# Kernel optimization log

Hardware: AMD Instinct MI355X
Metric: run time of the kernel (lower is better)

## Reference

```python
import jax, jax.numpy as jnp
import numpy as np

C = 256       # in_channels
IC = 128      # inter_channels = C // 2
G = 4         # num_group
D = IC // G   # per-group channels = 32
B, H, W_ = 4, 56, 56
EPS = 1e-5


def conv1x1(x, w, b=None):
    # x: (B,Cin,H,W), w: (Cout,Cin)
    y = jnp.einsum('bchw,oc->bohw', x, w)
    if b is not None:
        y = y + b[None, :, None, None]
    return y


def bn(x, scale, bias, mean, var):
    inv = scale / jnp.sqrt(var + EPS)
    return x * inv[None, :, None, None] + (bias - mean * inv)[None, :, None, None]


def setup_inputs():
    key = jax.random.key(0)
    ks = jax.random.split(key, 16)
    r = lambda k, shape, s=0.05: jax.random.normal(k, shape, jnp.float32) * s
    C4 = C // 4
    return {
        'x': jax.random.normal(ks[0], (B, C, H, W_), jnp.float32),
        'g_w': r(ks[1], (IC, C)), 'g_b': r(ks[2], (IC,)),
        'theta_w': r(ks[3], (IC, C)), 'theta_b': r(ks[4], (IC,)),
        'phi_w': r(ks[5], (IC, C)), 'phi_b': r(ks[6], (IC,)),
        'W_w': r(ks[7], (C, IC)), 'W_b': r(ks[8], (C,)),
        'bnW_scale': jnp.ones((C,)), 'bnW_bias': jnp.zeros((C,)),
        'bnW_mean': jnp.zeros((C,)), 'bnW_var': jnp.ones((C,)),
        'ff1_w': r(ks[9], (C4, C)),
        'ffbn1_scale': jnp.ones((C4,)), 'ffbn1_bias': jnp.zeros((C4,)),
        'ffbn1_mean': jnp.zeros((C4,)), 'ffbn1_var': jnp.ones((C4,)),
        'ff2_w': r(ks[10], (C4, C4, 3, 3)),
        'ffbn2_scale': jnp.ones((C4,)), 'ffbn2_bias': jnp.zeros((C4,)),
        'ffbn2_mean': jnp.zeros((C4,)), 'ffbn2_var': jnp.ones((C4,)),
        'ff3_w': r(ks[11], (C, C4)),
        'ffbn3_scale': jnp.ones((C,)), 'ffbn3_bias': jnp.zeros((C,)),
        'ffbn3_mean': jnp.zeros((C,)), 'ffbn3_var': jnp.ones((C,)),
    }


def reference(x, g_w, g_b, theta_w, theta_b, phi_w, phi_b, W_w, W_b,
              bnW_scale, bnW_bias, bnW_mean, bnW_var,
              ff1_w, ffbn1_scale, ffbn1_bias, ffbn1_mean, ffbn1_var,
              ff2_w, ffbn2_scale, ffbn2_bias, ffbn2_mean, ffbn2_var,
              ff3_w, ffbn3_scale, ffbn3_bias, ffbn3_mean, ffbn3_var):
    b, c, h, w = x.shape
    n = h * w
    # grouped non-local attention: channels split into G groups of D
    gx = conv1x1(x, g_w, g_b).reshape(b, G, D, n)       # (B,G,D,N)
    tx = conv1x1(x, theta_w, theta_b).reshape(b, G, D, n)
    px = conv1x1(x, phi_w, phi_b).reshape(b, G, D, n)
    f = jnp.einsum('bgdn,bgdm->bgnm', tx, px)           # (B,G,N,N) scores
    attn = jax.nn.softmax(f, axis=-1)                   # softmax over keys (torch dim=2 on (b,N,N))
    yy = jnp.einsum('bgnm,bgdm->bgdn', attn, gx)        # (B,G,D,N)
    y_out = yy.reshape(b, IC, h, w)
    W_y = bn(conv1x1(y_out, W_w, W_b), bnW_scale, bnW_bias, bnW_mean, bnW_var)
    z = jax.nn.relu(W_y + x)
    # FPNFFConv bottleneck FFN (BN in eval mode)
    o = jax.nn.relu(bn(conv1x1(z, ff1_w), ffbn1_scale, ffbn1_bias, ffbn1_mean, ffbn1_var))
    o = jax.lax.conv_general_dilated(o, ff2_w, (1, 1), 'SAME',
                                     dimension_numbers=('NCHW', 'OIHW', 'NCHW'))
    o = jax.nn.relu(bn(o, ffbn2_scale, ffbn2_bias, ffbn2_mean, ffbn2_var))
    o = bn(conv1x1(o, ff3_w), ffbn3_scale, ffbn3_bias, ffbn3_mean, ffbn3_var)
    return jax.nn.relu(o + z)
```

## Files before the change

kernel.cpp:

```cpp
#include <hip/hip_runtime.h>
#include <hip/hip_bf16.h>

#define NPIX 3136
#define BB 4
#define NSPLIT 5
#define LOG2E 1.4426950408889634f
#define ZLS 264

typedef unsigned short u16;
typedef __bf16 bf16x8 __attribute__((ext_vector_type(8)));
typedef float f32x4 __attribute__((ext_vector_type(4)));

__device__ __forceinline__ float b2f(u16 u) {
  union { unsigned u; float f; } c; c.u = ((unsigned)u) << 16; return c.f;
}
__device__ __forceinline__ u16 f2b(float f) {
  __hip_bfloat16 h = __float2bfloat16(f);
  return *reinterpret_cast<u16*>(&h);
}
__device__ __forceinline__ unsigned pk2(float a, float b) {
  return (unsigned)f2b(a) | ((unsigned)f2b(b) << 16);
}
__device__ __forceinline__ f32x4 mfma(bf16x8 a, bf16x8 b, f32x4 c) {
  return __builtin_amdgcn_mfma_f32_16x16x32_bf16(a, b, c, 0, 0, 0);
}
__device__ __forceinline__ float fast_exp2(float x) {
#if __has_builtin(__builtin_amdgcn_exp2f)
  return __builtin_amdgcn_exp2f(x);
#else
  float r; asm("v_exp_f32 %0, %1" : "=v"(r) : "v"(x)); return r;
#endif
}

template<int NSTEP, int NOT>
__device__ __forceinline__ void mf_gemm2(const u16* __restrict__ A0,
                                         const u16* __restrict__ A1,
                                         const u16* __restrict__ Brow, int sB,
                                         int lq, f32x4* acc) {
#pragma unroll
  for (int s = 0; s < NSTEP; ++s) {
    bf16x8 bf[NOT];
#pragma unroll
    for (int ot = 0; ot < NOT; ++ot)
      bf[ot] = *(const bf16x8*)(Brow + (size_t)ot * 16 * sB + s * 32 + lq * 8);
    bf16x8 a0 = *(const bf16x8*)(A0 + s * 32 + lq * 8);
    bf16x8 a1 = *(const bf16x8*)(A1 + s * 32 + lq * 8);
#pragma unroll
    for (int ot = 0; ot < NOT; ++ot) {
      acc[ot] = mfma(a0, bf[ot], acc[ot]);
      acc[NOT + ot] = mfma(a1, bf[ot], acc[NOT + ot]);
    }
  }
}

__global__ __launch_bounds__(256) void prep_w(
    const float* __restrict__ gw, const float* __restrict__ tw,
    const float* __restrict__ pw, const float* __restrict__ Ww,
    const float* __restrict__ f1w, const float* __restrict__ f2w,
    const float* __restrict__ f3w,
    u16* __restrict__ gwb, u16* __restrict__ twb, u16* __restrict__ pwb,
    u16* __restrict__ Wwb, u16* __restrict__ f1b, u16* __restrict__ f3b,
    u16* __restrict__ f2p) {
  for (int i = blockIdx.x * 256 + threadIdx.x; i < 200704; i += gridDim.x * 256) {
    int j = i;
    if (j < 32768) { gwb[j] = f2b(gw[j]); continue; } j -= 32768;
    if (j < 32768) { twb[j] = f2b(tw[j] * LOG2E); continue; } j -= 32768;
    if (j < 32768) { pwb[j] = f2b(pw[j]); continue; } j -= 32768;
    if (j < 32768) { Wwb[j] = f2b(Ww[j]); continue; } j -= 32768;
    if (j < 16384) { f1b[j] = f2b(f1w[j]); continue; } j -= 16384;
    if (j < 16384) { f3b[j] = f2b(f3w[j]); continue; } j -= 16384;
    int t = j >> 12, rem = j & 4095, co = rem >> 6, ci = rem & 63;
    f2p[j] = f2b(f2w[(co * 64 + ci) * 9 + t]);
  }
}

__global__ __launch_bounds__(256) void prep_x(const float* __restrict__ x,
                                              u16* __restrict__ xt) {
  __shared__ u16 sT[64 * 65];
  const int b = blockIdx.z, c0 = blockIdx.y * 64, n0 = blockIdx.x * 64;
  const int t = threadIdx.x;
#pragma unroll
  for (int cc = 0; cc < 4; ++cc) {
    int c = cc * 16 + (t >> 4), n4 = (t & 15) * 4;
    float4 v = *(const float4*)(x + ((size_t)(b * 256 + c0 + c)) * NPIX + n0 + n4);
    sT[c * 65 + n4 + 0] = f2b(v.x);
    sT[c * 65 + n4 + 1] = f2b(v.y);
    sT[c * 65 + n4 + 2] = f2b(v.z);
    sT[c * 65 + n4 + 3] = f2b(v.w);
  }
  __syncthreads();
#pragma unroll
  for (int nn = 0; nn < 4; ++nn) {
    int n = nn * 16 + (t >> 4), c4 = (t & 15) * 4;
    uint2 s;
    s.x = (unsigned)sT[(c4 + 0) * 65 + n] | ((unsigned)sT[(c4 + 1) * 65 + n] << 16);
    s.y = (unsigned)sT[(c4 + 2) * 65 + n] | ((unsigned)sT[(c4 + 3) * 65 + n] << 16);
    *(uint2*)(xt + ((size_t)b * NPIX + n0 + n) * 256 + c0 + c4) = s;
  }
}

__global__ __launch_bounds__(256) void proj_kernel(
    const u16* __restrict__ xt,
    const u16* __restrict__ gwb, const u16* __restrict__ twb, const u16* __restrict__ pwb,
    const float* __restrict__ gb, const float* __restrict__ tb, const float* __restrict__ pb,
    u16* __restrict__ gx, u16* __restrict__ Tq, u16* __restrict__ Pk) {
  const int b = blockIdx.z, oc = blockIdx.y, nb = blockIdx.x * 128;
  const int sec = oc >> 1, rbase = (oc & 1) * 64;
  const u16* wsel = sec == 0 ? gwb : (sec == 1 ? twb : pwb);
  const float* bsel = sec == 0 ? gb : (sec == 1 ? tb : pb);
  const int wv = threadIdx.x >> 6, lane = threadIdx.x & 63;
  const int lr = lane & 15, lq = lane >> 4;
  const int nrow0 = nb + wv * 32, nrow1 = nrow0 + 16;
  const int r0 = nrow0 + lr < NPIX ? nrow0 + lr : NPIX - 1;
  const int r1 = nrow1 + lr < NPIX ? nrow1 + lr : NPIX - 1;
  f32x4 acc[8] = {};
  mf_gemm2<8, 4>(xt + ((size_t)b * NPIX + r0) * 256,
                 xt + ((size_t)b * NPIX + r1) * 256,
                 wsel + (size_t)(rbase + lr) * 256, 256, lq, acc);
#pragma unroll
  for (int t = 0; t < 2; ++t) {
    const int qn = (t ? nrow1 : nrow0) + lq * 4;
    if (qn >= NPIX) continue;
#pragma unroll
    for (int ot = 0; ot < 4; ++ot) {
      const f32x4 a = acc[t * 4 + ot];
      const int o = rbase + ot * 16 + lr;
      float bias = bsel[o];
      if (sec == 1) bias *= LOG2E;
      if (sec == 0) {
        uint2 s;
        s.x = pk2(a[0] + bias, a[1] + bias);
        s.y = pk2(a[2] + bias, a[3] + bias);
        *(uint2*)(gx + ((size_t)b * 128 + o) * NPIX + qn) = s;
      } else {
        const int g = o >> 5, dl = o & 31;
        u16* dst = sec == 1 ? Tq : Pk;
        size_t base = (size_t)(b * 4 + g) * NPIX;
#pragma unroll
        for (int r = 0; r < 4; ++r)
          dst[(base + qn + r) * 32 + dl] = f2b(a[r] + bias);
      }
    }
  }
}

__global__ __launch_bounds__(256) void attn_kernel(
    const u16* __restrict__ Tq, const u16* __restrict__ Pk,
    const u16* __restrict__ gx, u16* __restrict__ OPb, float* __restrict__ LP) {
  __shared__ __align__(16) u16 Plds[4][32][40];
  const int bid = blockIdx.x;
  const int ks = bid / 400, rem = bid % 400;
  const int bg = rem / 25, qblk = rem % 25;
  const int b = bg >> 2, g = bg & 3;
  const int wave = threadIdx.x >> 6, lane = threadIdx.x & 63;
  const int lr = lane & 15, lq = lane >> 4;
  const int qbase = qblk * 128 + wave * 32;
  const int kc0 = ((ks * 98) / NSPLIT) * 32;
  const int kc1 = (((ks + 1) * 98) / NSPLIT) * 32;
  const u16* Qp = Tq + (size_t)bg * NPIX * 32;
  const u16* Kp = Pk + (size_t)bg * NPIX * 32;
  const u16* Vp = gx + ((size_t)b * 128 + g * 32) * NPIX;

  bf16x8 qf[2];
#pragma unroll
  for (int qi = 0; qi < 2; ++qi) {
    int row = qbase + qi * 16 + lr;
    row = row < NPIX ? row : NPIX - 1;
    qf[qi] = *(const bf16x8*)(Qp + (size_t)row * 32 + lq * 8);
  }
  const f32x4 z4 = {0.f, 0.f, 0.f, 0.f};
  f32x4 O[2][2], Lf[2];
#pragma unroll
  for (int qi = 0; qi < 2; ++qi) { O[qi][0] = z4; O[qi][1] = z4; Lf[qi] = z4; }
  bf16x8 onef;
#pragma unroll
  for (int j = 0; j < 8; ++j) onef[j] = (__bf16)1.0f;

#pragma unroll 1
  for (int kc = kc0; kc < kc1; kc += 32) {
    bf16x8 kf0 = *(const bf16x8*)(Kp + (size_t)(kc + lr) * 32 + lq * 8);
    bf16x8 kf1 = *(const bf16x8*)(Kp + (size_t)(kc + 16 + lr) * 32 + lq * 8);
    f32x4 St[2][2];
    St[0][0] = mfma(kf0, qf[0], z4);
    St[0][1] = mfma(kf0, qf[1], z4);
    St[1][0] = mfma(kf1, qf[0], z4);
    St[1][1] = mfma(kf1, qf[1], z4);
#pragma unroll
    for (int kt = 0; kt < 2; ++kt)
#pragma unroll
      for (int qi = 0; qi < 2; ++qi) {
        const f32x4 s = St[kt][qi];
        unsigned e0 = __builtin_bit_cast(unsigned, fast_exp2(s[0]));
        unsigned e1 = __builtin_bit_cast(unsigned, fast_exp2(s[1]));
        unsigned e2 = __builtin_bit_cast(unsigned, fast_exp2(s[2]));
        unsigned e3 = __builtin_bit_cast(unsigned, fast_exp2(s[3]));
        uint2 pk;
        pk.x = __builtin_amdgcn_perm(e1, e0, 0x07060302u);
        pk.y = __builtin_amdgcn_perm(e3, e2, 0x07060302u);
        *(uint2*)(&Plds[wave][qi * 16 + lr][kt * 16 + lq * 4]) = pk;
      }
    bf16x8 pf0 = *(const bf16x8*)(&Plds[wave][lr][lq * 8]);
    bf16x8 pf1 = *(const bf16x8*)(&Plds[wave][16 + lr][lq * 8]);
    bf16x8 vf0 = *(const bf16x8*)(Vp + (size_t)lr * NPIX + kc + lq * 8);
    bf16x8 vf1 = *(const bf16x8*)(Vp + (size_t)(16 + lr) * NPIX + kc + lq * 8);
    O[0][0] = mfma(pf0, vf0, O[0][0]);
    O[0][1] = mfma(pf0, vf1, O[0][1]);
    O[1][0] = mfma(pf1, vf0, O[1][0]);
    O[1][1] = mfma(pf1, vf1, O[1][1]);
    Lf[0] = mfma(pf0, onef, Lf[0]);
    Lf[1] = mfma(pf1, onef, Lf[1]);
  }
  const size_t sbase = (size_t)(ks * 16 + bg) * NPIX;
#pragma unroll
  for (int qi = 0; qi < 2; ++qi) {
#pragma unroll
    for (int r = 0; r < 4; ++r) {
      int qrow = qbase + qi * 16 + lq * 4 + r;
      if (qrow < NPIX) {
        size_t ob = (sbase + qrow) * 32;
        OPb[ob + lr] = f2b(O[qi][0][r]);
        OPb[ob + 16 + lr] = f2b(O[qi][1][r]);
        if (lr == 0) LP[sbase + qrow] = Lf[qi][r];
      }
    }
  }
}

__global__ __launch_bounds__(512) void wz_kernel(
    const u16* __restrict__ OPb, const float* __restrict__ LP,
    const u16* __restrict__ Wwb, const float* __restrict__ Wb,
    const float* __restrict__ sc, const float* __restrict__ bi,
    const float* __restrict__ mu, const float* __restrict__ var,
    const float* __restrict__ x,
    const u16* __restrict__ f1b, const float* __restrict__ s1,
    const float* __restrict__ b1, const float* __restrict__ m1,
    const float* __restrict__ v1,
    u16* __restrict__ zt, u16* __restrict__ o1t) {
  __shared__ float Ls[4][32];
  __shared__ __align__(16) u16 zl[32 * ZLS];
  const int b = blockIdx.y, nb = blockIdx.x * 32;
  const int tid = threadIdx.x;
  if (tid < 128) {
    int g = tid >> 5, row = tid & 31;
    float l = 0.f;
#pragma unroll
    for (int ks = 0; ks < NSPLIT; ++ks)
      l += LP[(size_t)(ks * 16 + b * 4 + g) * NPIX + nb + row];
    Ls[g][row] = 1.0f / l;
  }
  __syncthreads();
  const int wave = tid >> 6, lane = tid & 63;
  const int lr = lane & 15, lq = lane >> 4;
  const int oc = wave & 3, tt = wave >> 2;
  const int nrow = nb + tt * 16;
  f32x4 acc[4][4] = {};
#pragma unroll
  for (int g = 0; g < 4; ++g) {
    bf16x8 bf[4];
#pragma unroll
    for (int ot = 0; ot < 4; ++ot)
      bf[ot] = *(const bf16x8*)(Wwb + (size_t)(oc * 64 + ot * 16 + lr) * 128 + g * 32 + lq * 8);
#pragma unroll
    for (int ks = 0; ks < NSPLIT; ++ks) {
      bf16x8 af = *(const bf16x8*)(OPb +
          ((size_t)(ks * 16 + b * 4 + g) * NPIX + nrow + lr) * 32 + lq * 8);
#pragma unroll
      for (int ot = 0; ot < 4; ++ot)
        acc[g][ot] = mfma(af, bf[ot], acc[g][ot]);
    }
  }
#pragma unroll
  for (int ot = 0; ot < 4; ++ot) {
    const int o = oc * 64 + ot * 16 + lr;
    float inv = sc[o] * rsqrtf(var[o] + 1e-5f);
    float off = bi[o] - mu[o] * inv + Wb[o] * inv;
    const int qn = nrow + lq * 4;
    float4 xr = *(const float4*)(x + ((size_t)b * 256 + o) * NPIX + qn);
    float xv[4] = {xr.x, xr.y, xr.z, xr.w};
#pragma unroll
    for (int r = 0; r < 4; ++r) {
      int row = tt * 16 + lq * 4 + r;
      float y = acc[0][ot][r] * Ls[0][row] + acc[1][ot][r] * Ls[1][row] +
                acc[2][ot][r] * Ls[2][row] + acc[3][ot][r] * Ls[3][row];
      float v = fmaxf(y * inv + off + xv[r], 0.f);
      u16 vb = f2b(v);
      zt[((size_t)b * NPIX + qn + r) * 256 + o] = vb;
      zl[row * ZLS + o] = vb;
    }
  }
  __syncthreads();
  const int oc2 = wave & 3, tt2 = wave >> 2;
  f32x4 a1 = {0.f, 0.f, 0.f, 0.f};
  const u16* Bw = f1b + (size_t)(oc2 * 16 + lr) * 256;
#pragma unroll
  for (int s = 0; s < 8; ++s) {
    bf16x8 a0 = *(const bf16x8*)(&zl[(tt2 * 16 + lr) * ZLS + s * 32 + lq * 8]);
    bf16x8 bw = *(const bf16x8*)(Bw + s * 32 + lq * 8);
    a1 = mfma(a0, bw, a1);
  }
  const int o1 = oc2 * 16 + lr;
  float inv1 = s1[o1] * rsqrtf(v1[o1] + 1e-5f);
  float off1 = b1[o1] - m1[o1] * inv1;
  const int pr = nb + tt2 * 16 + lq * 4;
#pragma unroll
  for (int r = 0; r < 4; ++r) {
    float v = fmaxf(a1[r] * inv1 + off1, 0.f);
    o1t[((size_t)b * NPIX + pr + r) * 64 + o1] = f2b(v);
  }
}

__global__ __launch_bounds__(256) void ff2_kernel(
    const u16* __restrict__ o1t, const u16* __restrict__ f2p,
    const float* __restrict__ sc, const float* __restrict__ bi,
    const float* __restrict__ mu, const float* __restrict__ var,
    u16* __restrict__ o2t) {
  const int b = blockIdx.z, oc = blockIdx.y, nb = blockIdx.x * 128;
  const int wv = threadIdx.x >> 6, lane = threadIdx.x & 63;
  const int lr = lane & 15, lq = lane >> 4;
  const int n0 = nb + wv * 32 + lr, n1 = n0 + 16;
  const int h0 = n0 / 56, w0 = n0 % 56;
  const int h1 = n1 / 56, w1 = n1 % 56;
  f32x4 acc[4] = {};
#pragma unroll
  for (int t = 0; t < 9; ++t) {
    const int dh = t / 3 - 1, dw = t % 3 - 1;
    const bool v0 = (h0 + dh) >= 0 && (h0 + dh) < 56 && (w0 + dw) >= 0 && (w0 + dw) < 56;
    const bool v1 = (h1 + dh) >= 0 && (h1 + dh) < 56 && (w1 + dw) >= 0 && (w1 + dw) < 56;
    const u16* A0 = o1t + ((size_t)b * NPIX + n0 + dh * 56 + dw) * 64;
    const u16* A1 = o1t + ((size_t)b * NPIX + n1 + dh * 56 + dw) * 64;
    const u16* Br = f2p + (size_t)t * 4096 + (size_t)(oc * 32 + lr) * 64;
#pragma unroll
    for (int k2 = 0; k2 < 2; ++k2) {
      bf16x8 bf0 = *(const bf16x8*)(Br + k2 * 32 + lq * 8);
      bf16x8 bf1 = *(const bf16x8*)(Br + (size_t)16 * 64 + k2 * 32 + lq * 8);
      bf16x8 a0 = {}, a1 = {};
      if (v0) a0 = *(const bf16x8*)(A0 + k2 * 32 + lq * 8);
      if (v1) a1 = *(const bf16x8*)(A1 + k2 * 32 + lq * 8);
      acc[0] = mfma(a0, bf0, acc[0]);
      acc[1] = mfma(a0, bf1, acc[1]);
      acc[2] = mfma(a1, bf0, acc[2]);
      acc[3] = mfma(a1, bf1, acc[3]);
    }
  }
  const int nrow0 = nb + wv * 32;
#pragma unroll
  for (int t = 0; t < 2; ++t) {
    const int qn = nrow0 + t * 16 + lq * 4;
    if (qn >= NPIX) continue;
#pragma unroll
    for (int ot = 0; ot < 2; ++ot) {
      const f32x4 a = acc[t * 2 + ot];
      const int o = oc * 32 + ot * 16 + lr;
      float inv = sc[o] * rsqrtf(var[o] + 1e-5f);
      float off = bi[o] - mu[o] * inv;
#pragma unroll
      for (int r = 0; r < 4; ++r) {
        float v = fmaxf(a[r] * inv + off, 0.f);
        o2t[((size_t)b * NPIX + qn + r) * 64 + o] = f2b(v);
      }
    }
  }
}

__global__ __launch_bounds__(256) void ff3_kernel(
    const u16* __restrict__ o2t, const u16* __restrict__ f3b,
    const float* __restrict__ sc, const float* __restrict__ bi,
    const float* __restrict__ mu, const float* __restrict__ var,
    const u16* __restrict__ zt, float* __restrict__ out) {
  const int b = blockIdx.z, oc = blockIdx.y, nb = blockIdx.x * 128;
  const int wv = threadIdx.x >> 6, lane = threadIdx.x & 63;
  const int lr = lane & 15, lq = lane >> 4;
  const int nrow0 = nb + wv * 32, nrow1 = nrow0 + 16;
  const int r0 = nrow0 + lr < NPIX ? nrow0 + lr : NPIX - 1;
  const int r1 = nrow1 + lr < NPIX ? nrow1 + lr : NPIX - 1;
  f32x4 acc[8] = {};
  mf_gemm2<2, 4>(o2t + ((size_t)b * NPIX + r0) * 64,
                 o2t + ((size_t)b * NPIX + r1) * 64,
                 f3b + (size_t)(oc * 64 + lr) * 64, 64, lq, acc);
#pragma unroll
  for (int t = 0; t < 2; ++t) {
    const int qn = (t ? nrow1 : nrow0) + lq * 4;
    if (qn >= NPIX) continue;
#pragma unroll
    for (int ot = 0; ot < 4; ++ot) {
      const f32x4 a = acc[t * 4 + ot];
      const int o = oc * 64 + ot * 16 + lr;
      float inv = sc[o] * rsqrtf(var[o] + 1e-5f);
      float off = bi[o] - mu[o] * inv;
      float4 s;
      float* sv = (float*)&s;
#pragma unroll
      for (int r = 0; r < 4; ++r) {
        float zres = b2f(zt[((size_t)b * NPIX + qn + r) * 256 + o]);
        sv[r] = fmaxf(a[r] * inv + off + zres, 0.f);
      }
      *(float4*)(out + ((size_t)b * 256 + o) * NPIX + qn) = s;
    }
  }
}

extern "C" void kernel_launch(void* const* d_in, const int* in_sizes, int n_in,
                              void* d_out, int out_size, void* d_ws, size_t ws_size,
                              hipStream_t stream) {
  const float* x    = (const float*)d_in[0];
  const float* gw   = (const float*)d_in[1];
  const float* gb   = (const float*)d_in[2];
  const float* tw   = (const float*)d_in[3];
  const float* tb   = (const float*)d_in[4];
  const float* pw   = (const float*)d_in[5];
  const float* pb   = (const float*)d_in[6];
  const float* Ww   = (const float*)d_in[7];
  const float* Wb   = (const float*)d_in[8];
  const float* bnWs = (const float*)d_in[9];
  const float* bnWb = (const float*)d_in[10];
  const float* bnWm = (const float*)d_in[11];
  const float* bnWv = (const float*)d_in[12];
  const float* f1w  = (const float*)d_in[13];
  const float* b1s  = (const float*)d_in[14];
  const float* b1b  = (const float*)d_in[15];
  const float* b1m  = (const float*)d_in[16];
  const float* b1v  = (const float*)d_in[17];
  const float* f2w  = (const float*)d_in[18];
  const float* b2s  = (const float*)d_in[19];
  const float* b2b  = (const float*)d_in[20];
  const float* b2m  = (const float*)d_in[21];
  const float* b2v  = (const float*)d_in[22];
  const float* f3w  = (const float*)d_in[23];
  const float* b3s  = (const float*)d_in[24];
  const float* b3b  = (const float*)d_in[25];
  const float* b3m  = (const float*)d_in[26];
  const float* b3v  = (const float*)d_in[27];
  float* out = (float*)d_out;

  u16* p = (u16*)d_ws;
  u16* xt  = p; p += (size_t)BB * NPIX * 256;
  u16* gwb = p; p += 128 * 256;
  u16* twb = p; p += 128 * 256;
  u16* pwb = p; p += 128 * 256;
  u16* Wwb = p; p += 256 * 128;
  u16* f1b = p; p += 64 * 256;
  u16* f3b = p; p += 256 * 64;
  u16* f2p = p; p += 9 * 64 * 64;
  u16* Tq  = p; p += (size_t)16 * NPIX * 32;
  u16* Pk  = p; p += (size_t)16 * NPIX * 32;
  u16* gx  = p; p += (size_t)BB * 128 * NPIX;
  u16* OPb = p; p += (size_t)7 * 16 * NPIX * 32;
  float* LP = (float*)p; p += (size_t)7 * 16 * NPIX * 2;
  u16* zt  = p; p += (size_t)BB * NPIX * 256;
  u16* o1t = p; p += (size_t)BB * NPIX * 64;
  u16* o2t = p; p += (size_t)BB * NPIX * 64;

  prep_w<<<dim3(196), 256, 0, stream>>>(gw, tw, pw, Ww, f1w, f2w, f3w,
                                        gwb, twb, pwb, Wwb, f1b, f3b, f2p);
  prep_x<<<dim3(49, 4, BB), 256, 0, stream>>>(x, xt);
  proj_kernel<<<dim3(25, 6, BB), 256, 0, stream>>>(xt, gwb, twb, pwb, gb, tb, pb,
                                                   gx, Tq, Pk);
  attn_kernel<<<dim3(NSPLIT * 400), 256, 0, stream>>>(Tq, Pk, gx, OPb, LP);
  wz_kernel<<<dim3(98, BB), 512, 0, stream>>>(OPb, LP, Wwb, Wb,
                                              bnWs, bnWb, bnWm, bnWv, x,
                                              f1b, b1s, b1b, b1m, b1v,
                                              zt, o1t);
  ff2_kernel<<<dim3(25, 2, BB), 256, 0, stream>>>(o1t, f2p, b2s, b2b, b2m, b2v, o2t);
  ff3_kernel<<<dim3(25, 4, BB), 256, 0, stream>>>(o2t, f3b, b3s, b3b, b3m, b3v, zt, out);
}
```

Before: 238.3 us.

## Fuse 3x3 conv and final 1x1 conv into one kernel via LDS staging

Merges the ff2 (3x3 conv) and ff3 (1x1 conv plus residual) kernels into one 512-thread kernel. The ff2 output tile stays in shared memory as bf16 instead of round-tripping through global memory, which also removes one launch. Each block now computes all 64 ff2 output channels for 128 pixels, so the grid shrinks from 200 and 400 blocks to 100 blocks. That cuts parallelism and may leave many CUs idle.

```diff
diff --git a/kernel.cpp b/kernel.cpp
--- a/kernel.cpp
+++ b/kernel.cpp
@@ -309,92 +309,90 @@
   }
 }
 
-__global__ __launch_bounds__(256) void ff2_kernel(
+__global__ __launch_bounds__(512) void ff23_kernel(
     const u16* __restrict__ o1t, const u16* __restrict__ f2p,
-    const float* __restrict__ sc, const float* __restrict__ bi,
-    const float* __restrict__ mu, const float* __restrict__ var,
-    u16* __restrict__ o2t) {
-  const int b = blockIdx.z, oc = blockIdx.y, nb = blockIdx.x * 128;
-  const int wv = threadIdx.x >> 6, lane = threadIdx.x & 63;
+    const float* __restrict__ s2, const float* __restrict__ b2,
+    const float* __restrict__ m2, const float* __restrict__ v2,
+    const u16* __restrict__ f3b,
+    const float* __restrict__ s3, const float* __restrict__ b3,
+    const float* __restrict__ m3, const float* __restrict__ v3,
+    const u16* __restrict__ zt, float* __restrict__ out) {
+  __shared__ __align__(16) u16 o2l[128 * 72];
+  const int b = blockIdx.y, nb = blockIdx.x * 128;
+  const int tid = threadIdx.x;
+  const int wave = tid >> 6, lane = tid & 63;
   const int lr = lane & 15, lq = lane >> 4;
-  const int n0 = nb + wv * 32 + lr, n1 = n0 + 16;
-  const int h0 = n0 / 56, w0 = n0 % 56;
-  const int h1 = n1 / 56, w1 = n1 % 56;
-  f32x4 acc[4] = {};
-#pragma unroll
-  for (int t = 0; t < 9; ++t) {
-    const int dh = t / 3 - 1, dw = t % 3 - 1;
-    const bool v0 = (h0 + dh) >= 0 && (h0 + dh) < 56 && (w0 + dw) >= 0 && (w0 + dw) < 56;
-    const bool v1 = (h1 + dh) >= 0 && (h1 + dh) < 56 && (w1 + dw) >= 0 && (w1 + dw) < 56;
-    const u16* A0 = o1t + ((size_t)b * NPIX + n0 + dh * 56 + dw) * 64;
-    const u16* A1 = o1t + ((size_t)b * NPIX + n1 + dh * 56 + dw) * 64;
-    const u16* Br = f2p + (size_t)t * 4096 + (size_t)(oc * 32 + lr) * 64;
-#pragma unroll
-    for (int k2 = 0; k2 < 2; ++k2) {
-      bf16x8 bf0 = *(const bf16x8*)(Br + k2 * 32 + lq * 8);
-      bf16x8 bf1 = *(const bf16x8*)(Br + (size_t)16 * 64 + k2 * 32 + lq * 8);
-      bf16x8 a0 = {}, a1 = {};
-      if (v0) a0 = *(const bf16x8*)(A0 + k2 * 32 + lq * 8);
-      if (v1) a1 = *(const bf16x8*)(A1 + k2 * 32 + lq * 8);
-      acc[0] = mfma(a0, bf0, acc[0]);
-      acc[1] = mfma(a0, bf1, acc[1]);
-      acc[2] = mfma(a1, bf0, acc[2]);
-      acc[3] = mfma(a1, bf1, acc[3]);
-    }
-  }
-  const int nrow0 = nb + wv * 32;
-#pragma unroll
-  for (int t = 0; t < 2; ++t) {
-    const int qn = nrow0 + t * 16 + lq * 4;
-    if (qn >= NPIX) continue;
-#pragma unroll
-    for (int ot = 0; ot < 2; ++ot) {
-      const f32x4 a = acc[t * 2 + ot];
-      const int o = oc * 32 + ot * 16 + lr;
-      float inv = sc[o] * rsqrtf(var[o] + 1e-5f);
-      float off = bi[o] - mu[o] * inv;
+  {
+    const int n0 = nb + wave * 16 + lr;
+    const int n0c = n0 < NPIX ? n0 : NPIX - 1;
+    const int h0 = n0c / 56, w0 = n0c % 56;
+    f32x4 acc2[4] = {};
+#pragma unroll
+    for (int t = 0; t < 9; ++t) {
+      const int dh = t / 3 - 1, dw = t % 3 - 1;
+      const bool v0 = n0 < NPIX && (h0 + dh) >= 0 && (h0 + dh) < 56 &&
+                      (w0 + dw) >= 0 && (w0 + dw) < 56;
+      const u16* A0 = o1t + ((size_t)b * NPIX + n0c + dh * 56 + dw) * 64;
+      const u16* Br = f2p + (size_t)t * 4096 + (size_t)lr * 64;
+#pragma unroll
+      for (int k2 = 0; k2 < 2; ++k2) {
+        bf16x8 a0 = {};
+        if (v0) a0 = *(const bf16x8*)(A0 + k2 * 32 + lq * 8);
+#pragma unroll
+        for (int ot = 0; ot < 4; ++ot) {
+          bf16x8 bf = *(const bf16x8*)(Br + (size_t)ot * 16 * 64 + k2 * 32 + lq * 8);
+          acc2[ot] = mfma(a0, bf, acc2[ot]);
+        }
+      }
+    }
+#pragma unroll
+    for (int ot = 0; ot < 4; ++ot) {
+      const int o = ot * 16 + lr;
+      float inv = s2[o] * rsqrtf(v2[o] + 1e-5f);
+      float off = b2[o] - m2[o] * inv;
 #pragma unroll
       for (int r = 0; r < 4; ++r) {
-        float v = fmaxf(a[r] * inv + off, 0.f);
-        o2t[((size_t)b * NPIX + qn + r) * 64 + o] = f2b(v);
-      }
-    }
-  }
-}
-
-__global__ __launch_bounds__(256) void ff3_kernel(
-    const u16* __restrict__ o2t, const u16* __restrict__ f3b,
-    const float* __restrict__ sc, const float* __restrict__ bi,
-    const float* __restrict__ mu, const float* __restrict__ var,
-    const u16* __restrict__ zt, float* __restrict__ out) {
-  const int b = blockIdx.z, oc = blockIdx.y, nb = blockIdx.x * 128;
-  const int wv = threadIdx.x >> 6, lane = threadIdx.x & 63;
-  const int lr = lane & 15, lq = lane >> 4;
-  const int nrow0 = nb + wv * 32, nrow1 = nrow0 + 16;
-  const int r0 = nrow0 + lr < NPIX ? nrow0 + lr : NPIX - 1;
-  const int r1 = nrow1 + lr < NPIX ? nrow1 + lr : NPIX - 1;
-  f32x4 acc[8] = {};
-  mf_gemm2<2, 4>(o2t + ((size_t)b * NPIX + r0) * 64,
-                 o2t + ((size_t)b * NPIX + r1) * 64,
-                 f3b + (size_t)(oc * 64 + lr) * 64, 64, lq, acc);
-#pragma unroll
-  for (int t = 0; t < 2; ++t) {
-    const int qn = (t ? nrow1 : nrow0) + lq * 4;
-    if (qn >= NPIX) continue;
+        float v = fmaxf(acc2[ot][r] * inv + off, 0.f);
+        o2l[(wave * 16 + lq * 4 + r) * 72 + o] = f2b(v);
+      }
+    }
+  }
+  __syncthreads();
+  const int oc3 = wave & 3, tt3 = wave >> 2;
+  bf16x8 bf3[4][2];
+#pragma unroll
+  for (int ot = 0; ot < 4; ++ot)
+#pragma unroll
+    for (int s = 0; s < 2; ++s)
+      bf3[ot][s] = *(const bf16x8*)(f3b +
+          (size_t)(oc3 * 64 + ot * 16 + lr) * 64 + s * 32 + lq * 8);
+#pragma unroll
+  for (int rt = 0; rt < 4; ++rt) {
+    const int lrow = tt3 * 64 + rt * 16;
+    bf16x8 a0 = *(const bf16x8*)(&o2l[(lrow + lr) * 72 + lq * 8]);
+    bf16x8 a1 = *(const bf16x8*)(&o2l[(lrow + lr) * 72 + 32 + lq * 8]);
+    f32x4 acc3[4] = {};
 #pragma unroll
     for (int ot = 0; ot < 4; ++ot) {
-      const f32x4 a = acc[t * 4 + ot];
-      const int o = oc * 64 + ot * 16 + lr;
-      float inv = sc[o] * rsqrtf(var[o] + 1e-5f);
-      float off = bi[o] - mu[o] * inv;
-      float4 s;
-      float* sv = (float*)&s;
-#pragma unroll
-      for (int r = 0; r < 4; ++r) {
-        float zres = b2f(zt[((size_t)b * NPIX + qn + r) * 256 + o]);
-        sv[r] = fmaxf(a[r] * inv + off + zres, 0.f);
-      }
-      *(float4*)(out + ((size_t)b * 256 + o) * NPIX + qn) = s;
+      acc3[ot] = mfma(a0, bf3[ot][0], acc3[ot]);
+      acc3[ot] = mfma(a1, bf3[ot][1], acc3[ot]);
+    }
+    const int qn = nb + lrow + lq * 4;
+    if (qn < NPIX) {
+#pragma unroll
+      for (int ot = 0; ot < 4; ++ot) {
+        const int o = oc3 * 64 + ot * 16 + lr;
+        float inv = s3[o] * rsqrtf(v3[o] + 1e-5f);
+        float off = b3[o] - m3[o] * inv;
+        float4 sv4;
+        float* sv = (float*)&sv4;
+#pragma unroll
+        for (int r = 0; r < 4; ++r) {
+          float zres = b2f(zt[((size_t)b * NPIX + qn + r) * 256 + o]);
+          sv[r] = fmaxf(acc3[ot][r] * inv + off + zres, 0.f);
+        }
+        *(float4*)(out + ((size_t)b * 256 + o) * NPIX + qn) = sv4;
+      }
     }
   }
 }
@@ -449,6 +447,7 @@
   u16* zt  = p; p += (size_t)BB * NPIX * 256;
   u16* o1t = p; p += (size_t)BB * NPIX * 64;
   u16* o2t = p; p += (size_t)BB * NPIX * 64;
+  (void)o2t;
 
   prep_w<<<dim3(196), 256, 0, stream>>>(gw, tw, pw, Ww, f1w, f2w, f3w,
                                         gwb, twb, pwb, Wwb, f1b, f3b, f2p);
@@ -460,6 +459,7 @@
                                               bnWs, bnWb, bnWm, bnWv, x,
                                               f1b, b1s, b1b, b1m, b1v,
                                               zt, o1t);
-  ff2_kernel<<<dim3(25, 2, BB), 256, 0, stream>>>(o1t, f2p, b2s, b2b, b2m, b2v, o2t);
-  ff3_kernel<<<dim3(25, 4, BB), 256, 0, stream>>>(o2t, f3b, b3s, b3b, b3m, b3v, zt, out);
-}
+  ff23_kernel<<<dim3(25, BB), 512, 0, stream>>>(o1t, f2p, b2s, b2b, b2m, b2v,
+                                                f3b, b3s, b3b, b3m, b3v,
+                                                zt, out);
+}
```

Result: slower. 251.3 us (+5.4%).
